# Optimization experiments

Hardware: AMD Instinct MI355X
Metric: run time of the kernel (lower is better)

The kernel has to match this reference:

```python
import jax, jax.numpy as jnp
import numpy as np

ALIGNED_H = 7
ALIGNED_W = 7
SPATIAL_SCALE = 0.0625


def setup_inputs() -> dict:
    key = jax.random.key(0)
    k1, k2, k3, k4, k5, k6 = jax.random.split(key, 6)
    N, C, FH, FW = 4, 256, 100, 152
    R = 4000
    features = jax.random.normal(k1, (N, C, FH, FW), dtype=jnp.float32)
    x1 = jax.random.uniform(k2, (R,), minval=0.0, maxval=1800.0)
    y1 = jax.random.uniform(k3, (R,), minval=0.0, maxval=1200.0)
    bw = jax.random.uniform(k4, (R,), minval=16.0, maxval=400.0)
    bh = jax.random.uniform(k5, (R,), minval=16.0, maxval=300.0)
    rois = jnp.stack([x1, y1, x1 + bw, y1 + bh], axis=1).astype(jnp.float32)
    bids = jax.random.randint(k6, (R,), 0, N, dtype=jnp.int32)
    return {"features": features, "rois": rois, "bids": bids}


def _roi_align(features, rois, bids, AH, AW, scale):
    # features: [N,C,FH,FW]; rois: [R,4]; bids: [R] -> [R,C,AH,AW]
    N, C, FH, FW = features.shape
    r = rois * scale
    x1, y1, x2, y2 = r[:, 0], r[:, 1], r[:, 2], r[:, 3]
    bin_w = jnp.clip(x2 - x1 + 1.0, 0.0) / (AW - 1)
    bin_h = jnp.clip(y2 - y1 + 1.0, 0.0) / (AH - 1)
    h = y1[:, None] + jnp.arange(AH, dtype=features.dtype) * bin_h[:, None]  # [R,AH]
    w = x1[:, None] + jnp.arange(AW, dtype=features.dtype) * bin_w[:, None]  # [R,AW]
    valid_h = (h >= 0) & (h < FH)
    valid_w = (w >= 0) & (w < FW)
    hs = jnp.clip(jnp.floor(h), 0.0, FH - 2).astype(jnp.int32)  # [R,AH]
    ws = jnp.clip(jnp.floor(w), 0.0, FW - 2).astype(jnp.int32)  # [R,AW]
    hr = (h - hs)[:, :, None, None]  # [R,AH,1,1]
    wr = (w - ws)[:, None, :, None]  # [R,1,AW,1]
    b = bids[:, None, None]            # [R,1,1]
    hi = hs[:, :, None]                # [R,AH,1]
    wi = ws[:, None, :]                # [R,1,AW]
    def gather(dh, dw):
        # advanced indexing -> [R,AH,AW,C]
        return features[b, :, hi + dh, wi + dw]
    val = (gather(0, 0) * (1 - hr) * (1 - wr)
           + gather(0, 1) * (1 - hr) * wr
           + gather(1, 0) * hr * (1 - wr)
           + gather(1, 1) * hr * wr)
    mask = (valid_h[:, :, None] & valid_w[:, None, :])[:, :, :, None]
    val = jnp.where(mask, val, 0.0)
    return jnp.transpose(val, (0, 3, 1, 2))  # [R,C,AH,AW]


def reference(features, rois, bids):
    # RoIAlign on (aligned+1)^2 grid, then 2x2 stride-1 average pool -> 7x7
    x = _roi_align(features, rois, bids, ALIGNED_H + 1, ALIGNED_W + 1, SPATIAL_SCALE)
    out = (x[:, :, :-1, :-1] + x[:, :, :-1, 1:]
           + x[:, :, 1:, :-1] + x[:, :, 1:, 1:]) * 0.25
    return out
```

## Files before the change

### kernel.cpp

```cpp
#include <hip/hip_runtime.h>

#define N_IMG 4
#define C_CH  256
#define FH    100
#define FW    152
#define CHW   (C_CH * FH * FW)
#define OUT_PER_ROI (C_CH * 7 * 7)
#define SCALE 0.0625f
#define ROW_BYTES (FW * C_CH * 4)
#define CH_BYTES  (C_CH * 4)
#define CPAD 260

typedef float f4 __attribute__((ext_vector_type(4)));

__global__ __launch_bounds__(256) void transpose_nchw_nhwc(
    const float* __restrict__ in, float* __restrict__ out) {
  const int x0 = blockIdx.x * 32;
  const int y  = blockIdx.y;
  const int b  = blockIdx.z;
  __shared__ float tile[32][C_CH + 1];
  const int chl = threadIdx.x & 31;
  const int xq  = threadIdx.x >> 5;
  const int x   = x0 + xq * 4;
  const bool inb = (x < FW);
  const float4* src4 = (const float4*)in;
#pragma unroll
  for (int cc = 0; cc < C_CH; cc += 32) {
    const int ch = cc + chl;
    float4 v = make_float4(0.f, 0.f, 0.f, 0.f);
    if (inb) v = src4[((size_t)b * C_CH + ch) * (FH * FW / 4) + y * (FW / 4) + (x >> 2)];
    tile[xq * 4 + 0][ch] = v.x;
    tile[xq * 4 + 1][ch] = v.y;
    tile[xq * 4 + 2][ch] = v.z;
    tile[xq * 4 + 3][ch] = v.w;
  }
  __syncthreads();
  const int ch = threadIdx.x;
  float* dst = out + (((size_t)b * FH + y) * FW) * C_CH + ch;
#pragma unroll
  for (int xi = 0; xi < 32; ++xi) {
    const int xx = x0 + xi;
    if (xx < FW) dst[(size_t)xx * C_CH] = tile[xi][ch];
  }
}

__global__ __launch_bounds__(512, 4) void roialign_nhwc(
    const float* __restrict__ feat, const float* __restrict__ rois,
    const int* __restrict__ bids, float* __restrict__ out) {
  const int r  = blockIdx.x;
  const int cg = threadIdx.x & 63;
  const int i  = threadIdx.x >> 6;
  __shared__ float smp[64 * CPAD];

  const float x1 = rois[r * 4 + 0] * SCALE;
  const float y1 = rois[r * 4 + 1] * SCALE;
  const float x2 = rois[r * 4 + 2] * SCALE;
  const float y2 = rois[r * 4 + 3] * SCALE;
  const int   b  = bids[r];
  const float bw = fmaxf(x2 - x1 + 1.0f, 0.0f) * (1.0f / 7.0f);
  const float bh = fmaxf(y2 - y1 + 1.0f, 0.0f) * (1.0f / 7.0f);

  const float h   = y1 + (float)i * bh;
  const float hsf = fminf(fmaxf(floorf(h), 0.0f), (float)(FH - 2));
  const float hr  = h - hsf;
  const float mh  = (h >= 0.0f && h < (float)FH) ? 1.0f : 0.0f;
  const float a0  = (1.0f - hr) * mh;
  const float a1  = hr * mh;

  const char* fbb  = (const char*)(feat + (size_t)b * CHW);
  const int   row0 = (int)hsf * ROW_BYTES + cg * 16;

  float* lbase = &smp[(i * 8) * CPAD + cg * 4];

#pragma unroll
  for (int j = 0; j < 8; ++j) {
    const float w   = x1 + (float)j * bw;
    const float wsf = fminf(fmaxf(floorf(w), 0.0f), (float)(FW - 2));
    const float wr  = w - wsf;
    const float mw  = (w >= 0.0f && w < (float)FW) ? 1.0f : 0.0f;
    const float q0  = (1.0f - wr) * mw;
    const float q1  = wr * mw;
    const int   o0  = row0 + (int)wsf * CH_BYTES;
    const f4 g00 = *(const f4*)(fbb + o0);
    const f4 g01 = *(const f4*)(fbb + o0 + CH_BYTES);
    const f4 g10 = *(const f4*)(fbb + o0 + ROW_BYTES);
    const f4 g11 = *(const f4*)(fbb + o0 + ROW_BYTES + CH_BYTES);
    const f4 s = (g00 * q0 + g01 * q1) * a0 + (g10 * q0 + g11 * q1) * a1;
    *(f4*)(lbase + j * CPAD) = s;
  }

  __syncthreads();

  f4* dst = (f4*)(out + (size_t)r * OUT_PER_ROI);
  const int g0 = (int)threadIdx.x * 4;
  int c   = (g0 * 669) >> 15;
  int rem = g0 - c * 49;
#pragma unroll
  for (int k = 0; k < 7; ++k) {
    const int idx = (int)threadIdx.x + k * 512;
    if (idx < (OUT_PER_ROI / 4)) {
      f4 v;
      int cc = c, rr = rem;
#pragma unroll
      for (int e = 0; e < 4; ++e) {
        const int p    = (rr * 37) >> 8;
        const int j    = rr - p * 7;
        const int base = (p * 8 + j) * CPAD + cc;
        v[e] = (smp[base] + smp[base + CPAD] +
                smp[base + 8 * CPAD] + smp[base + 9 * CPAD]) * 0.25f;
        if (++rr == 49) { rr = 0; ++cc; }
      }
      __builtin_nontemporal_store(v, dst + idx);
    }
    rem += 39; c += 41;
    if (rem >= 49) { rem -= 49; ++c; }
  }
}

extern "C" void kernel_launch(void* const* d_in, const int* in_sizes, int n_in,
                              void* d_out, int out_size, void* d_ws, size_t ws_size,
                              hipStream_t stream) {
  (void)n_in; (void)out_size; (void)ws_size;
  const float* features = (const float*)d_in[0];
  const float* rois     = (const float*)d_in[1];
  const int*   bids     = (const int*)d_in[2];
  float* out = (float*)d_out;
  const int R = in_sizes[1] / 4;

  float* nhwc = (float*)d_ws;
  dim3 tgrid((FW + 31) / 32, FH, N_IMG);
  transpose_nchw_nhwc<<<tgrid, 256, 0, stream>>>(features, nhwc);
  roialign_nhwc<<<R, 512, 0, stream>>>(nhwc, rois, bids, out);
}
```

Before: 334.7 us.

## Bin ROIs spatially per XCD for cache locality and vectorize transpose stores

Adds a single-block kernel that counting-sorts ROIs by image and an 8x8 spatial cell of their centre. The RoIAlign grid maps block IDs so that each of the 8 round-robin XCD slots processes a contiguous run of the sorted order, so neighbouring ROIs share feature rows in the per-XCD L2. The transpose kernel also switches to float4 LDS reads and global stores with a padded tile. This adds a serial single-block sort launch, and the scatter within each bin is nondeterministic, which changes only the processing order, not the results.

Result: faster. 296.6 us (-11.4%).

```diff
diff --git a/kernel.cpp b/kernel.cpp
--- a/kernel.cpp
+++ b/kernel.cpp
@@ -13,12 +13,44 @@
 
 typedef float f4 __attribute__((ext_vector_type(4)));
 
+__global__ __launch_bounds__(256) void bin_rois(
+    const float* __restrict__ rois, const int* __restrict__ bids, int R,
+    int* __restrict__ order) {
+  __shared__ int hist[256];
+  __shared__ int base[256];
+  for (int k = threadIdx.x; k < 256; k += 256) hist[k] = 0;
+  __syncthreads();
+  for (int r = threadIdx.x; r < R; r += 256) {
+    const float cx = (rois[r * 4 + 0] + rois[r * 4 + 2]) * 0.5f * SCALE;
+    const float cy = (rois[r * 4 + 1] + rois[r * 4 + 3]) * 0.5f * SCALE;
+    int xb = (int)(cx * (8.0f / FW)); xb = xb < 0 ? 0 : (xb > 7 ? 7 : xb);
+    int yb = (int)(cy * (8.0f / FH)); yb = yb < 0 ? 0 : (yb > 7 ? 7 : yb);
+    const int key = (bids[r] << 6) | (yb << 3) | xb;
+    atomicAdd(&hist[key], 1);
+  }
+  __syncthreads();
+  if (threadIdx.x == 0) {
+    int s = 0;
+    for (int k = 0; k < 256; ++k) { base[k] = s; s += hist[k]; }
+  }
+  __syncthreads();
+  for (int r = threadIdx.x; r < R; r += 256) {
+    const float cx = (rois[r * 4 + 0] + rois[r * 4 + 2]) * 0.5f * SCALE;
+    const float cy = (rois[r * 4 + 1] + rois[r * 4 + 3]) * 0.5f * SCALE;
+    int xb = (int)(cx * (8.0f / FW)); xb = xb < 0 ? 0 : (xb > 7 ? 7 : xb);
+    int yb = (int)(cy * (8.0f / FH)); yb = yb < 0 ? 0 : (yb > 7 ? 7 : yb);
+    const int key = (bids[r] << 6) | (yb << 3) | xb;
+    const int pos = atomicAdd(&base[key], 1);
+    order[pos] = r;
+  }
+}
+
 __global__ __launch_bounds__(256) void transpose_nchw_nhwc(
     const float* __restrict__ in, float* __restrict__ out) {
   const int x0 = blockIdx.x * 32;
   const int y  = blockIdx.y;
   const int b  = blockIdx.z;
-  __shared__ float tile[32][C_CH + 1];
+  __shared__ float tile[32][C_CH + 4];
   const int chl = threadIdx.x & 31;
   const int xq  = threadIdx.x >> 5;
   const int x   = x0 + xq * 4;
@@ -35,19 +67,25 @@
     tile[xq * 4 + 3][ch] = v.w;
   }
   __syncthreads();
-  const int ch = threadIdx.x;
-  float* dst = out + (((size_t)b * FH + y) * FW) * C_CH + ch;
+  const int chg = threadIdx.x & 63;
+  const int xs  = threadIdx.x >> 6;
+  float* dstB = out + (((size_t)b * FH + y) * FW) * C_CH;
 #pragma unroll
-  for (int xi = 0; xi < 32; ++xi) {
-    const int xx = x0 + xi;
-    if (xx < FW) dst[(size_t)xx * C_CH] = tile[xi][ch];
+  for (int xi = 0; xi < 32; xi += 4) {
+    const int xx = x0 + xi + xs;
+    if (xx < FW) {
+      const f4 v = *(const f4*)&tile[xi + xs][chg * 4];
+      *(f4*)(dstB + (size_t)xx * C_CH + chg * 4) = v;
+    }
   }
 }
 
 __global__ __launch_bounds__(512, 4) void roialign_nhwc(
     const float* __restrict__ feat, const float* __restrict__ rois,
-    const int* __restrict__ bids, float* __restrict__ out) {
-  const int r  = blockIdx.x;
+    const int* __restrict__ bids, const int* __restrict__ order,
+    int R, float* __restrict__ out) {
+  const int g  = blockIdx.x;
+  const int r  = order[((R & 7) == 0) ? ((g & 7) * (R >> 3) + (g >> 3)) : g];
   const int cg = threadIdx.x & 63;
   const int i  = threadIdx.x >> 6;
   __shared__ float smp[64 * CPAD];
@@ -127,8 +165,11 @@
   float* out = (float*)d_out;
   const int R = in_sizes[1] / 4;
 
-  float* nhwc = (float*)d_ws;
+  float* nhwc  = (float*)d_ws;
+  int*   order = (int*)((char*)d_ws + (64u << 20));
+
+  bin_rois<<<1, 256, 0, stream>>>(rois, bids, R, order);
   dim3 tgrid((FW + 31) / 32, FH, N_IMG);
   transpose_nchw_nhwc<<<tgrid, 256, 0, stream>>>(features, nhwc);
-  roialign_nhwc<<<R, 512, 0, stream>>>(nhwc, rois, bids, out);
+  roialign_nhwc<<<R, 512, 0, stream>>>(nhwc, rois, bids, order, R, out);
 }
```
